# Performance work log

Hardware: AMD Instinct MI355X
Metric: run time of the kernel (lower is better)

## Reference

```python
import jax, jax.numpy as jnp
import numpy as np

N = 50000      # n_nodes
E = 800000     # n_edges (nnz)
F = 256        # n_features
H = 256        # architecture (GCN hidden)
K = 16         # n_clusters
CLUSTER_REG = 1.0
CON_REG = 1.0


def setup_inputs() -> dict:
    key = jax.random.key(0)
    ks = jax.random.split(key, 12)
    inp = {
        "edge_src": jax.random.randint(ks[0], (E,), 0, N, dtype=jnp.int32),
        "edge_dst": jax.random.randint(ks[1], (E,), 0, N, dtype=jnp.int32),
        "edge_w_norm": jax.random.uniform(ks[2], (E,), dtype=jnp.float32),
        "features": jax.random.normal(ks[3], (N, F), dtype=jnp.float32),
        "aug_features": jax.random.normal(ks[4], (N, F), dtype=jnp.float32),
        # GCN encoder params (Linear no-bias + additive bias per DGI-style GCN)
        "W1": jax.random.normal(ks[5], (F, H), dtype=jnp.float32) / np.sqrt(F),
        "b1": jnp.zeros((H,), dtype=jnp.float32),
        # student GCN params
        "Ws": jax.random.normal(ks[6], (H, K), dtype=jnp.float32) / np.sqrt(H),
        "bs": jnp.zeros((K,), dtype=jnp.float32),
        # teacher GCN params (EMA copy; fixed here)
        "Wt": jax.random.normal(ks[7], (H, K), dtype=jnp.float32) / np.sqrt(H),
        "bt": jnp.zeros((K,), dtype=jnp.float32),
        "n_nodes": N,
    }
    return inp


def _spmm(w, src, dst, X, n):
    # (sparse A) @ X with A given as COO (src=row, dst=col, w=value)
    return jax.ops.segment_sum(w[:, None] * X[dst], src, num_segments=n)


def _gcn(X, W, b, w, src, dst, n):
    # act(spmm(A_norm, X @ W) + b) with act = selu
    return jax.nn.selu(_spmm(w, src, dst, X @ W, n) + b)


def _normalize(x):
    # F.normalize(x, dim=-1, p=2)
    nrm = jnp.sqrt(jnp.sum(x * x, axis=-1, keepdims=True))
    return x / jnp.maximum(nrm, 1e-12)


def reference(edge_src, edge_dst, edge_w_norm, features, aug_features,
              W1, b1, Ws, bs, Wt, bt, n_nodes):
    n = features.shape[0]
    n_edges = edge_src.shape[0]

    # encoder + student assignments
    gcn_out = _gcn(features, W1, b1, edge_w_norm, edge_src, edge_dst, n)
    logits = _spmm(edge_w_norm, edge_src, edge_dst, gcn_out @ Ws, n) + bs
    assignments = jax.nn.softmax(jax.nn.selu(logits), axis=1)  # [N, K]

    # degrees = torch.sparse.sum(graph, dim=0) (binary adjacency values)
    ones_e = jnp.ones((n_edges,), dtype=features.dtype)
    degrees = jax.ops.segment_sum(ones_e, edge_dst, num_segments=n)[:, None]  # [N,1]

    # graph_pooled = (A @ S).T @ S  (A values are all 1)
    AS = jax.ops.segment_sum(assignments[edge_dst], edge_src, num_segments=n)
    graph_pooled = AS.T @ assignments  # [K, K]

    normalizer_left = assignments.T @ degrees          # [K, 1]
    normalizer = (normalizer_left @ normalizer_left.T) / 2.0 / n_edges
    spectral_loss = -jnp.trace(graph_pooled - normalizer) / 2.0 / n_edges

    cluster_sizes = jnp.sum(assignments, axis=0)
    cluster_loss = (jnp.linalg.norm(cluster_sizes) / n_nodes * np.sqrt(float(K)) - 1.0)
    cluster_loss = cluster_loss * CLUSTER_REG

    # teacher branch (no grad)
    g2 = _gcn(aug_features, W1, b1, edge_w_norm, edge_src, edge_dst, n)
    t_logits = _spmm(edge_w_norm, edge_src, edge_dst, g2 @ Wt, n) + bt
    assignments_hat = jax.lax.stop_gradient(
        jax.nn.softmax(jax.nn.selu(t_logits), axis=-1))

    con = jnp.mean(2.0 - 2.0 * jnp.sum(_normalize(assignments_hat) * _normalize(assignments), axis=-1))

    loss = spectral_loss + cluster_loss + CON_REG * con
    return loss
```

## Files before the change

kernel.cpp:

```cpp
#include <hip/hip_runtime.h>
#include <math.h>

constexpr int Fdim = 256;
constexpr int Hdim = 256;
constexpr int Kc   = 16;

constexpr int RSTRIDE = 32;
constexpr int NRED    = 34;
constexpr int BCAP    = 5120;

typedef __attribute__((ext_vector_type(8))) short s8v;
typedef __attribute__((ext_vector_type(4))) float f4v;

__device__ __forceinline__ float selu1(float x){
    const float scale = 1.0507009873554805f;
    const float alpha = 1.6732632423543772f;
    return scale * (x > 0.f ? x : alpha * expm1f(x));
}

__device__ __forceinline__ ushort f2bf(float x){
    union { float f; unsigned u; } c; c.f = x;
    unsigned r = c.u + 0x7fffu + ((c.u >> 16) & 1u);
    return (ushort)(r >> 16);
}

__device__ __forceinline__ float bflo(unsigned v){
    union { unsigned u; float f; } c; c.u = v << 16; return c.f;
}
__device__ __forceinline__ float bfhi(unsigned v){
    union { unsigned u; float f; } c; c.u = v & 0xffff0000u; return c.f;
}

__device__ __forceinline__ unsigned char f2fp8(float x){
    int v = __builtin_amdgcn_cvt_pk_fp8_f32(x, x, 0, false);
    return (unsigned char)(v & 0xff);
}

__global__ __launch_bounds__(256) void bin_kernel(
        const int* __restrict__ src, const int* __restrict__ dst,
        const float* __restrict__ w,
        int* __restrict__ bcnt,
        int* __restrict__ bsrc, uint2* __restrict__ bdw, int E, int nbuck){
    __shared__ int hist[256];
    __shared__ int base[256];
    __shared__ int cur[256];
    int t = threadIdx.x;
    int chunk = (E + gridDim.x - 1) / gridDim.x;
    int lo = blockIdx.x * chunk;
    int hi = min(lo + chunk, E);
    hist[t] = 0;
    __syncthreads();
    for (int i = lo + t; i < hi; i += 256)
        atomicAdd(&hist[src[i] >> 8], 1);
    __syncthreads();
    if (t < nbuck && hist[t] > 0)
        base[t] = atomicAdd(&bcnt[t * 32], hist[t]);
    cur[t] = 0;
    __syncthreads();
    for (int i = lo + t; i < hi; i += 256){
        int s = src[i], d = dst[i];
        float wv = w[i];
        int b = s >> 8;
        int p = base[b] + atomicAdd(&cur[b], 1);
        if (p < BCAP){
            bsrc[(size_t)b * BCAP + p] = s;
            bdw[(size_t)b * BCAP + p]  = make_uint2((unsigned)d, __float_as_uint(wv));
        }
    }
}

__global__ __launch_bounds__(256) void bbase_kernel(const int* __restrict__ bcnt,
        int* __restrict__ bbase, int* __restrict__ roff, int nbuck, int n){
    __shared__ int s[256];
    int t = threadIdx.x;
    int v = (t < nbuck) ? min(bcnt[t * 32], BCAP) : 0;
    s[t] = v;
    __syncthreads();
    for (int off = 1; off < 256; off <<= 1){
        int x = (t >= off) ? s[t - off] : 0;
        __syncthreads();
        s[t] += x;
        __syncthreads();
    }
    if (t < nbuck) bbase[t] = s[t] - v;
    if (t == 255) roff[n] = s[255];
}

__global__ __launch_bounds__(256) void csr_build_kernel(
        const int* __restrict__ bcnt, const int* __restrict__ bbase,
        const int* __restrict__ bsrc, const uint2* __restrict__ bdw,
        int* __restrict__ roff, uint2* __restrict__ csr, int n){
    __shared__ int hist[256];
    __shared__ int loc[256];
    __shared__ int cur[256];
    int b = blockIdx.x, t = threadIdx.x;
    int cnt  = min(bcnt[b * 32], BCAP);
    int base = bbase[b];
    hist[t] = 0;
    __syncthreads();
    for (int i = t; i < cnt; i += 256)
        atomicAdd(&hist[bsrc[(size_t)b * BCAP + i] & 255], 1);
    __syncthreads();
    int v = hist[t];
    loc[t] = v;
    __syncthreads();
    for (int off = 1; off < 256; off <<= 1){
        int x = (t >= off) ? loc[t - off] : 0;
        __syncthreads();
        loc[t] += x;
        __syncthreads();
    }
    int gi = b * 256 + t;
    if (gi < n) roff[gi] = base + loc[t] - v;
    cur[t] = 0;
    __syncthreads();
    for (int i = t; i < cnt; i += 256){
        int s   = bsrc[(size_t)b * BCAP + i];
        int idx = s & 255;
        int p = base + (loc[idx] - hist[idx]) + atomicAdd(&cur[idx], 1);
        csr[p] = bdw[(size_t)b * BCAP + i];
    }
}

__global__ void castw_kernel(const float* __restrict__ W, ushort* __restrict__ Wt){
    __shared__ float t[16][17];
    int tx = threadIdx.x, ty = threadIdx.y;
    int k  = blockIdx.y * 16 + ty;
    int nn = blockIdx.x * 16 + tx;
    t[ty][tx] = W[k * 256 + nn];
    __syncthreads();
    int n2 = blockIdx.x * 16 + ty;
    int k2 = blockIdx.y * 16 + tx;
    Wt[n2 * 256 + k2] = f2bf(t[tx][ty]);
}

__global__ void castwk_kernel(const float* __restrict__ Ws, const float* __restrict__ Wt,
                              ushort* __restrict__ WsT, ushort* __restrict__ WtT){
    int h = threadIdx.x;
    #pragma unroll
    for (int c = 0; c < 16; ++c){
        WsT[c * 256 + h] = f2bf(Ws[h * 16 + c]);
        WtT[c * 256 + h] = f2bf(Wt[h * 16 + c]);
    }
}

__global__ __launch_bounds__(256, 2) void gemm_xw_kernel(
        const float* __restrict__ A0, const float* __restrict__ A1,
        const ushort* __restrict__ Bt,
        unsigned char* __restrict__ C8, int M){
    __shared__ ushort blds[16384];
    int tid = threadIdx.x;
    int n0  = blockIdx.x * 128;
    int bm  = blockIdx.y * 128;
    const float* A = blockIdx.z ? A1 : A0;
    int halfoff = blockIdx.z * 256;

    int w = tid >> 6, l = tid & 63;
    int lr = l & 15, lk = l >> 4;

    int r0 = bm + w * 32 + lr;
    int r1 = r0 + 16;
    int rc0 = min(r0, M - 1), rc1 = min(r1, M - 1);

    f4v acc[2][8];
    #pragma unroll
    for (int m = 0; m < 2; ++m)
        #pragma unroll
        for (int t = 0; t < 8; ++t)
            acc[m][t] = (f4v){0.f, 0.f, 0.f, 0.f};

    for (int kp = 0; kp < 2; ++kp){
        #pragma unroll
        for (int j = 0; j < 8; ++j){
            int c  = j * 256 + tid;
            int nl = c >> 4, kc = c & 15;
            uint4 v = *reinterpret_cast<const uint4*>(
                Bt + (((size_t)(n0 + nl)) << 8) + kp * 128 + (kc << 3));
            unsigned boff = (unsigned)(((nl << 8) + (kc << 4)) ^ ((nl & 7) << 4));
            *reinterpret_cast<uint4*>(reinterpret_cast<char*>(blds) + boff) = v;
        }

        const float* a0 = A + (size_t)rc0 * 256 + kp * 128 + lk * 8;
        const float* a1 = A + (size_t)rc1 * 256 + kp * 128 + lk * 8;
        s8v af0[4], af1[4];
        #pragma unroll
        for (int ks = 0; ks < 4; ++ks){
            float4 x0 = *reinterpret_cast<const float4*>(a0 + ks * 32);
            float4 x1 = *reinterpret_cast<const float4*>(a0 + ks * 32 + 4);
            af0[ks][0] = (short)f2bf(x0.x); af0[ks][1] = (short)f2bf(x0.y);
            af0[ks][2] = (short)f2bf(x0.z); af0[ks][3] = (short)f2bf(x0.w);
            af0[ks][4] = (short)f2bf(x1.x); af0[ks][5] = (short)f2bf(x1.y);
            af0[ks][6] = (short)f2bf(x1.z); af0[ks][7] = (short)f2bf(x1.w);
            float4 y0 = *reinterpret_cast<const float4*>(a1 + ks * 32);
            float4 y1 = *reinterpret_cast<const float4*>(a1 + ks * 32 + 4);
            af1[ks][0] = (short)f2bf(y0.x); af1[ks][1] = (short)f2bf(y0.y);
            af1[ks][2] = (short)f2bf(y0.z); af1[ks][3] = (short)f2bf(y0.w);
            af1[ks][4] = (short)f2bf(y1.x); af1[ks][5] = (short)f2bf(y1.y);
            af1[ks][6] = (short)f2bf(y1.z); af1[ks][7] = (short)f2bf(y1.w);
        }
        __syncthreads();

        #pragma unroll
        for (int ks = 0; ks < 4; ++ks){
            #pragma unroll
            for (int t = 0; t < 8; ++t){
                int nl = t * 16 + lr;
                unsigned boff = (unsigned)(((nl << 8) + ((ks * 4 + lk) << 4)) ^ ((nl & 7) << 4));
                s8v bf = *reinterpret_cast<const s8v*>(reinterpret_cast<const char*>(blds) + boff);
                acc[0][t] = __builtin_amdgcn_mfma_f32_16x16x32_bf16(af0[ks], bf, acc[0][t], 0, 0, 0);
                acc[1][t] = __builtin_amdgcn_mfma_f32_16x16x32_bf16(af1[ks], bf, acc[1][t], 0, 0, 0);
            }
        }
        if (kp == 0) __syncthreads();
    }

    #pragma unroll
    for (int m = 0; m < 2; ++m){
        #pragma unroll
        for (int t = 0; t < 8; ++t){
            int col = n0 + t * 16 + lr;
            #pragma unroll
            for (int j = 0; j < 4; ++j){
                int row = bm + w * 32 + m * 16 + lk * 4 + j;
                if (row < M) C8[(size_t)row * 512 + halfoff + col] = f2fp8(acc[m][t][j]);
            }
        }
    }
}

__global__ __launch_bounds__(256) void spmm_h2_kernel(
        const unsigned char* __restrict__ XWp,
        const int* __restrict__ roff, const uint2* __restrict__ csr,
        const float* __restrict__ b1,
        ushort* __restrict__ Gs, ushort* __restrict__ Gt, int n){
    int wid = threadIdx.x >> 6, lane = threadIdx.x & 63;
    int r = blockIdx.x * 4 + wid;
    if (r >= n) return;
    int half = lane >> 5;
    int hl   = lane & 31;
    const unsigned char* base = XWp + lane * 8;
    int e0 = roff[r], e1 = roff[r + 1];
    float acc[8] = {};

    #define ACCUM8(V, W) do{                                                      \
        auto fa_ = __builtin_amdgcn_cvt_pk_f32_fp8((V).x, false);                 \
        acc[0] = fmaf((W), fa_[0], acc[0]); acc[1] = fmaf((W), fa_[1], acc[1]);   \
        auto fb_ = __builtin_amdgcn_cvt_pk_f32_fp8((V).x, true);                  \
        acc[2] = fmaf((W), fb_[0], acc[2]); acc[3] = fmaf((W), fb_[1], acc[3]);   \
        auto fc_ = __builtin_amdgcn_cvt_pk_f32_fp8((V).y, false);                 \
        acc[4] = fmaf((W), fc_[0], acc[4]); acc[5] = fmaf((W), fc_[1], acc[5]);   \
        auto fd_ = __builtin_amdgcn_cvt_pk_f32_fp8((V).y, true);                  \
        acc[6] = fmaf((W), fd_[0], acc[6]); acc[7] = fmaf((W), fd_[1], acc[7]);   \
    }while(0)

    int e = e0;
    for (; e + 7 < e1; e += 8){
        uint2 c0 = csr[e],     c1 = csr[e + 1];
        uint2 c2 = csr[e + 2], c3 = csr[e + 3];
        uint2 c4 = csr[e + 4], c5 = csr[e + 5];
        uint2 c6 = csr[e + 6], c7 = csr[e + 7];
        uint2 v0 = *reinterpret_cast<const uint2*>(base + ((size_t)c0.x << 9));
        uint2 v1 = *reinterpret_cast<const uint2*>(base + ((size_t)c1.x << 9));
        uint2 v2 = *reinterpret_cast<const uint2*>(base + ((size_t)c2.x << 9));
        uint2 v3 = *reinterpret_cast<const uint2*>(base + ((size_t)c3.x << 9));
        uint2 v4 = *reinterpret_cast<const uint2*>(base + ((size_t)c4.x << 9));
        uint2 v5 = *reinterpret_cast<const uint2*>(base + ((size_t)c5.x << 9));
        uint2 v6 = *reinterpret_cast<const uint2*>(base + ((size_t)c6.x << 9));
        uint2 v7 = *reinterpret_cast<const uint2*>(base + ((size_t)c7.x << 9));
        ACCUM8(v0, __uint_as_float(c0.y)); ACCUM8(v1, __uint_as_float(c1.y));
        ACCUM8(v2, __uint_as_float(c2.y)); ACCUM8(v3, __uint_as_float(c3.y));
        ACCUM8(v4, __uint_as_float(c4.y)); ACCUM8(v5, __uint_as_float(c5.y));
        ACCUM8(v6, __uint_as_float(c6.y)); ACCUM8(v7, __uint_as_float(c7.y));
    }
    for (; e + 3 < e1; e += 4){
        uint2 c0 = csr[e],     c1 = csr[e + 1];
        uint2 c2 = csr[e + 2], c3 = csr[e + 3];
        uint2 v0 = *reinterpret_cast<const uint2*>(base + ((size_t)c0.x << 9));
        uint2 v1 = *reinterpret_cast<const uint2*>(base + ((size_t)c1.x << 9));
        uint2 v2 = *reinterpret_cast<const uint2*>(base + ((size_t)c2.x << 9));
        uint2 v3 = *reinterpret_cast<const uint2*>(base + ((size_t)c3.x << 9));
        ACCUM8(v0, __uint_as_float(c0.y)); ACCUM8(v1, __uint_as_float(c1.y));
        ACCUM8(v2, __uint_as_float(c2.y)); ACCUM8(v3, __uint_as_float(c3.y));
    }
    for (; e < e1; ++e){
        uint2 c = csr[e];
        uint2 v = *reinterpret_cast<const uint2*>(base + ((size_t)c.x << 9));
        ACCUM8(v, __uint_as_float(c.y));
    }
    #undef ACCUM8

    const float* bp = b1 + hl * 8;
    float4 bb0 = *reinterpret_cast<const float4*>(bp);
    float4 bb1 = *reinterpret_cast<const float4*>(bp + 4);
    float bv[8] = {bb0.x, bb0.y, bb0.z, bb0.w, bb1.x, bb1.y, bb1.z, bb1.w};
    ushort o[8];
    #pragma unroll
    for (int q = 0; q < 8; ++q) o[q] = f2bf(selu1(acc[q] + bv[q]));
    uint4 ov = *reinterpret_cast<const uint4*>(o);
    ushort* gout = (half ? Gt : Gs) + (size_t)r * Hdim + hl * 8;
    *reinterpret_cast<uint4*>(gout) = ov;
}

__global__ __launch_bounds__(256) void gemm_k2_kernel(
        const ushort* __restrict__ Gs, const ushort* __restrict__ Gt,
        const ushort* __restrict__ WsT, const ushort* __restrict__ WtT,
        unsigned* __restrict__ GSp, int n){
    int wv = blockIdx.x * 4 + (threadIdx.x >> 6);
    int l  = threadIdx.x & 63;
    int lr = l & 15, lk = l >> 4;
    int nw = (n + 15) >> 4;
    if (wv >= nw) return;
    int r0 = wv * 16;

    s8v bs_[8], bt_[8];
    #pragma unroll
    for (int ks = 0; ks < 8; ++ks){
        bs_[ks] = *reinterpret_cast<const s8v*>(WsT + lr * 256 + ks * 32 + lk * 8);
        bt_[ks] = *reinterpret_cast<const s8v*>(WtT + lr * 256 + ks * 32 + lk * 8);
    }

    f4v accs = (f4v){0.f,0.f,0.f,0.f}, acct = (f4v){0.f,0.f,0.f,0.f};
    int row = min(r0 + lr, n - 1);
    const ushort* gsrow = Gs + (size_t)row * 256 + lk * 8;
    const ushort* gtrow = Gt + (size_t)row * 256 + lk * 8;
    #pragma unroll
    for (int ks = 0; ks < 8; ++ks){
        s8v a_s = *reinterpret_cast<const s8v*>(gsrow + ks * 32);
        s8v a_t = *reinterpret_cast<const s8v*>(gtrow + ks * 32);
        accs = __builtin_amdgcn_mfma_f32_16x16x32_bf16(a_s, bs_[ks], accs, 0, 0, 0);
        acct = __builtin_amdgcn_mfma_f32_16x16x32_bf16(a_t, bt_[ks], acct, 0, 0, 0);
    }
    #pragma unroll
    for (int j = 0; j < 4; ++j){
        int rr = r0 + lk * 4 + j;
        if (rr < n){
            unsigned pv = (unsigned)f2bf(accs[j]) | ((unsigned)f2bf(acct[j]) << 16);
            GSp[(size_t)rr * 16 + lr] = pv;
        }
    }
}

__global__ __launch_bounds__(256) void spmm_k2_kernel(
        const unsigned* __restrict__ GSp,
        const int* __restrict__ roff, const uint2* __restrict__ csr,
        const float* __restrict__ bsv, const float* __restrict__ btv,
        float* __restrict__ asg, float* __restrict__ red, int n){
    int tid  = threadIdx.x;
    int wid  = tid >> 6, lane = tid & 63;
    int slot = lane >> 4, j = lane & 15;
    float bs_ = bsv[j], bt_ = btv[j];
    float cs_l = 0.f, con_l = 0.f;

    int rstride = gridDim.x * 4;
    for (int r = blockIdx.x * 4 + wid; r < n; r += rstride){
        int e0 = roff[r], e1 = roff[r + 1];
        float as_ = 0.f, at_ = 0.f;
        for (int e = e0 + slot; e < e1; e += 4){
            uint2 c = csr[e];
            float w = __uint_as_float(c.y);
            unsigned v = GSp[(size_t)c.x * 16 + j];
            as_ = fmaf(w, bflo(v), as_);
            at_ = fmaf(w, bfhi(v), at_);
        }
        as_ += __shfl_xor(as_, 16); as_ += __shfl_xor(as_, 32);
        at_ += __shfl_xor(at_, 16); at_ += __shfl_xor(at_, 32);
        float xs = selu1(as_ + bs_);
        float xt = selu1(at_ + bt_);
        float ms = xs, mt = xt;
        #pragma unroll
        for (int off = 8; off >= 1; off >>= 1){
            ms = fmaxf(ms, __shfl_xor(ms, off));
            mt = fmaxf(mt, __shfl_xor(mt, off));
        }
        float es = expf(xs - ms), et = expf(xt - mt);
        float ss = es, st = et;
        #pragma unroll
        for (int off = 8; off >= 1; off >>= 1){
            ss += __shfl_xor(ss, off);
            st += __shfl_xor(st, off);
        }
        float a = es / ss, b = et / st;
        if (slot == 0) asg[(size_t)r * 16 + j] = a;
        cs_l += a;
        float dot = a * b, na = a * a, nb = b * b;
        #pragma unroll
        for (int off = 8; off >= 1; off >>= 1){
            dot += __shfl_xor(dot, off);
            na  += __shfl_xor(na, off);
            nb  += __shfl_xor(nb, off);
        }
        if (j == 0){
            na = fmaxf(sqrtf(na), 1e-12f);
            nb = fmaxf(sqrtf(nb), 1e-12f);
            con_l += 2.f - 2.f * dot / (na * nb);
        }
    }

    cs_l  += __shfl_xor(cs_l, 16);  cs_l  += __shfl_xor(cs_l, 32);  cs_l  *= 0.25f;
    con_l += __shfl_xor(con_l, 16); con_l += __shfl_xor(con_l, 32); con_l *= 0.25f;

    __shared__ float part[4][17];
    if (lane < 16) part[wid][lane] = cs_l;
    if (lane == 0) part[wid][16]   = con_l;
    __syncthreads();
    if (tid < 16){
        float s = part[0][tid] + part[1][tid] + part[2][tid] + part[3][tid];
        atomicAdd(&red[(16 + tid) * RSTRIDE], s);
    } else if (tid == 16){
        float s = part[0][16] + part[1][16] + part[2][16] + part[3][16];
        atomicAdd(&red[32 * RSTRIDE], s);
    }
}

__global__ __launch_bounds__(256) void edge_trace_kernel(const int* __restrict__ src,
        const int* __restrict__ dst, const float* __restrict__ as_,
        float* __restrict__ red, int E){
    int tid    = blockIdx.x * blockDim.x + threadIdx.x;
    int stride = gridDim.x * blockDim.x;
    float dot = 0.f;
    float nl[16] = {};
    for (int i = tid; i < E; i += stride){
        const float4* pa = reinterpret_cast<const float4*>(as_ + (size_t)src[i] * 16);
        const float4* pb = reinterpret_cast<const float4*>(as_ + (size_t)dst[i] * 16);
        #pragma unroll
        for (int q = 0; q < 4; ++q){
            float4 va = pa[q]; float4 vb = pb[q];
            dot = fmaf(va.x, vb.x, dot); dot = fmaf(va.y, vb.y, dot);
            dot = fmaf(va.z, vb.z, dot); dot = fmaf(va.w, vb.w, dot);
            nl[q*4+0] += vb.x; nl[q*4+1] += vb.y;
            nl[q*4+2] += vb.z; nl[q*4+3] += vb.w;
        }
    }
    #pragma unroll
    for (int off = 1; off < 64; off <<= 1){
        dot += __shfl_xor(dot, off);
        #pragma unroll
        for (int k = 0; k < 16; ++k) nl[k] += __shfl_xor(nl[k], off);
    }
    __shared__ float part[4][17];
    int wid = threadIdx.x >> 6, lane = threadIdx.x & 63;
    if (lane == 0){
        #pragma unroll
        for (int k = 0; k < 16; ++k) part[wid][k] = nl[k];
        part[wid][16] = dot;
    }
    __syncthreads();
    int t = threadIdx.x;
    if (t < 16){
        float s = part[0][t] + part[1][t] + part[2][t] + part[3][t];
        atomicAdd(&red[t * RSTRIDE], s);
    } else if (t == 16){
        float s = part[0][16] + part[1][16] + part[2][16] + part[3][16];
        atomicAdd(&red[33 * RSTRIDE], s);
    }
}

__global__ void finalize_kernel(const float* __restrict__ red, float* __restrict__ out,
                                int n, int E){
    float trace = red[33 * RSTRIDE];
    float nl2 = 0.f, cs2 = 0.f;
    #pragma unroll
    for (int k = 0; k < 16; ++k){
        nl2 = fmaf(red[k * RSTRIDE],        red[k * RSTRIDE],        nl2);
        cs2 = fmaf(red[(16 + k) * RSTRIDE], red[(16 + k) * RSTRIDE], cs2);
    }
    float twoE = 2.f * (float)E;
    float spectral = -(trace - nl2 / twoE) / twoE;
    float cluster  = sqrtf(cs2) / (float)n * 4.f - 1.f;
    float con      = red[32 * RSTRIDE] / (float)n;
    out[0] = spectral + cluster + con;
}

extern "C" void kernel_launch(void* const* d_in, const int* in_sizes, int n_in,
                              void* d_out, int out_size, void* d_ws, size_t ws_size,
                              hipStream_t stream){
    const int*   esrc = (const int*)d_in[0];
    const int*   edst = (const int*)d_in[1];
    const float* ew   = (const float*)d_in[2];
    const float* feat = (const float*)d_in[3];
    const float* faug = (const float*)d_in[4];
    const float* W1   = (const float*)d_in[5];
    const float* b1   = (const float*)d_in[6];
    const float* Wsm  = (const float*)d_in[7];
    const float* bsv  = (const float*)d_in[8];
    const float* Wtm  = (const float*)d_in[9];
    const float* btv  = (const float*)d_in[10];
    int E = in_sizes[0];
    int N = in_sizes[3] / Fdim;

    char* ws = (char*)d_ws;
    size_t off = 0;
    auto alloc = [&](size_t bytes) -> char* {
        char* p = ws + off;
        off = (off + bytes + 255) & ~(size_t)255;
        return p;
    };
    int nbuck = (N + 255) >> 8;
    unsigned char* XWp = (unsigned char*)alloc((size_t)N * 512);
    ushort*   Gs    = (ushort*)alloc((size_t)N * Hdim * 2);
    ushort*   Gt    = (ushort*)alloc((size_t)N * Hdim * 2);
    unsigned* GSp   = (unsigned*)alloc((size_t)N * Kc * 4);
    float*    ASG_S = (float*)alloc((size_t)N * Kc * 4);
    ushort*   WT    = (ushort*)alloc((size_t)256 * 256 * 2);
    ushort*   WsT   = (ushort*)alloc((size_t)16 * 256 * 2);
    ushort*   WtT   = (ushort*)alloc((size_t)16 * 256 * 2);
    int*      ROFF  = (int*)alloc((size_t)(N + 1) * 4);
    int*      BBASE = (int*)alloc((size_t)(nbuck + 1) * 4);
    int*      BCNT  = (int*)alloc((size_t)nbuck * 32 * 4);
    int*      BSRC  = (int*)alloc((size_t)nbuck * BCAP * 4);
    uint2*    BDW   = (uint2*)alloc((size_t)nbuck * BCAP * 8);
    uint2*    CSR8  = (uint2*)alloc((size_t)E * 8);
    float*    RED   = (float*)alloc((size_t)NRED * RSTRIDE * 4);

    hipMemsetAsync(BCNT, 0, (size_t)nbuck * 32 * 4, stream);
    hipMemsetAsync(RED, 0, (size_t)NRED * RSTRIDE * 4, stream);

    castw_kernel<<<dim3(16, 16), dim3(16, 16), 0, stream>>>(W1, WT);
    castwk_kernel<<<1, 256, 0, stream>>>(Wsm, Wtm, WsT, WtT);
    bin_kernel<<<256, 256, 0, stream>>>(esrc, edst, ew, BCNT, BSRC, BDW, E, nbuck);
    bbase_kernel<<<1, 256, 0, stream>>>(BCNT, BBASE, ROFF, nbuck, N);
    csr_build_kernel<<<nbuck, 256, 0, stream>>>(BCNT, BBASE, BSRC, BDW, ROFF, CSR8, N);

    dim3 gg(2, (N + 127) / 128, 2);
    gemm_xw_kernel<<<gg, 256, 0, stream>>>(feat, faug, WT, XWp, N);

    spmm_h2_kernel<<<(N + 3) / 4, 256, 0, stream>>>(XWp, ROFF, CSR8, b1, Gs, Gt, N);

    int nw = (N + 15) / 16;
    gemm_k2_kernel<<<(nw + 3) / 4, 256, 0, stream>>>(Gs, Gt, WsT, WtT, GSp, N);

    spmm_k2_kernel<<<2048, 256, 0, stream>>>(GSp, ROFF, CSR8, bsv, btv,
                                             ASG_S, RED, N);

    edge_trace_kernel<<<256, 256, 0, stream>>>(esrc, edst, ASG_S, RED, E);
    finalize_kernel<<<1, 1, 0, stream>>>(RED, (float*)d_out, N, E);
}
```

Before: 247.8 us.

## Merge edge binning with XW GEMM and fold bucket scan into CSR build

The two weight-cast kernels become one prep kernel. Edge binning and the feature GEMM now run as different block ranges of a single mega-kernel, so the bandwidth-bound binning can overlap with the MFMA GEMM. The bucket-base prefix scan is recomputed inside every CSR-build block, which removes a separate single-block kernel. This cuts the launch count from 6 to 3 in exchange for redundant scan work and a shared-memory footprint sized for the GEMM in all blocks.

```diff
diff --git a/kernel.cpp b/kernel.cpp
--- a/kernel.cpp
+++ b/kernel.cpp
@@ -36,124 +36,82 @@
     return (unsigned char)(v & 0xff);
 }
 
-__global__ __launch_bounds__(256) void bin_kernel(
-        const int* __restrict__ src, const int* __restrict__ dst,
-        const float* __restrict__ w,
-        int* __restrict__ bcnt,
-        int* __restrict__ bsrc, uint2* __restrict__ bdw, int E, int nbuck){
-    __shared__ int hist[256];
-    __shared__ int base[256];
-    __shared__ int cur[256];
+__global__ __launch_bounds__(256) void prep_kernel(
+        const float* __restrict__ W1, ushort* __restrict__ WT,
+        const float* __restrict__ Ws, const float* __restrict__ Wt,
+        ushort* __restrict__ WsT, ushort* __restrict__ WtT){
+    __shared__ float tbuf[16][17];
+    int b = blockIdx.x;
     int t = threadIdx.x;
-    int chunk = (E + gridDim.x - 1) / gridDim.x;
-    int lo = blockIdx.x * chunk;
-    int hi = min(lo + chunk, E);
-    hist[t] = 0;
-    __syncthreads();
-    for (int i = lo + t; i < hi; i += 256)
-        atomicAdd(&hist[src[i] >> 8], 1);
-    __syncthreads();
-    if (t < nbuck && hist[t] > 0)
-        base[t] = atomicAdd(&bcnt[t * 32], hist[t]);
-    cur[t] = 0;
-    __syncthreads();
-    for (int i = lo + t; i < hi; i += 256){
-        int s = src[i], d = dst[i];
-        float wv = w[i];
-        int b = s >> 8;
-        int p = base[b] + atomicAdd(&cur[b], 1);
-        if (p < BCAP){
-            bsrc[(size_t)b * BCAP + p] = s;
-            bdw[(size_t)b * BCAP + p]  = make_uint2((unsigned)d, __float_as_uint(wv));
-        }
-    }
-}
-
-__global__ __launch_bounds__(256) void bbase_kernel(const int* __restrict__ bcnt,
-        int* __restrict__ bbase, int* __restrict__ roff, int nbuck, int n){
-    __shared__ int s[256];
-    int t = threadIdx.x;
-    int v = (t < nbuck) ? min(bcnt[t * 32], BCAP) : 0;
-    s[t] = v;
-    __syncthreads();
-    for (int off = 1; off < 256; off <<= 1){
-        int x = (t >= off) ? s[t - off] : 0;
-        __syncthreads();
-        s[t] += x;
-        __syncthreads();
-    }
-    if (t < nbuck) bbase[t] = s[t] - v;
-    if (t == 255) roff[n] = s[255];
-}
-
-__global__ __launch_bounds__(256) void csr_build_kernel(
-        const int* __restrict__ bcnt, const int* __restrict__ bbase,
-        const int* __restrict__ bsrc, const uint2* __restrict__ bdw,
-        int* __restrict__ roff, uint2* __restrict__ csr, int n){
-    __shared__ int hist[256];
-    __shared__ int loc[256];
-    __shared__ int cur[256];
-    int b = blockIdx.x, t = threadIdx.x;
-    int cnt  = min(bcnt[b * 32], BCAP);
-    int base = bbase[b];
-    hist[t] = 0;
-    __syncthreads();
-    for (int i = t; i < cnt; i += 256)
-        atomicAdd(&hist[bsrc[(size_t)b * BCAP + i] & 255], 1);
-    __syncthreads();
-    int v = hist[t];
-    loc[t] = v;
-    __syncthreads();
-    for (int off = 1; off < 256; off <<= 1){
-        int x = (t >= off) ? loc[t - off] : 0;
-        __syncthreads();
-        loc[t] += x;
-        __syncthreads();
-    }
-    int gi = b * 256 + t;
-    if (gi < n) roff[gi] = base + loc[t] - v;
-    cur[t] = 0;
-    __syncthreads();
-    for (int i = t; i < cnt; i += 256){
-        int s   = bsrc[(size_t)b * BCAP + i];
-        int idx = s & 255;
-        int p = base + (loc[idx] - hist[idx]) + atomicAdd(&cur[idx], 1);
-        csr[p] = bdw[(size_t)b * BCAP + i];
-    }
-}
-
-__global__ void castw_kernel(const float* __restrict__ W, ushort* __restrict__ Wt){
-    __shared__ float t[16][17];
-    int tx = threadIdx.x, ty = threadIdx.y;
-    int k  = blockIdx.y * 16 + ty;
-    int nn = blockIdx.x * 16 + tx;
-    t[ty][tx] = W[k * 256 + nn];
-    __syncthreads();
-    int n2 = blockIdx.x * 16 + ty;
-    int k2 = blockIdx.y * 16 + tx;
-    Wt[n2 * 256 + k2] = f2bf(t[tx][ty]);
-}
-
-__global__ void castwk_kernel(const float* __restrict__ Ws, const float* __restrict__ Wt,
-                              ushort* __restrict__ WsT, ushort* __restrict__ WtT){
-    int h = threadIdx.x;
-    #pragma unroll
-    for (int c = 0; c < 16; ++c){
-        WsT[c * 256 + h] = f2bf(Ws[h * 16 + c]);
-        WtT[c * 256 + h] = f2bf(Wt[h * 16 + c]);
-    }
-}
-
-__global__ __launch_bounds__(256, 2) void gemm_xw_kernel(
+    if (b < 256){
+        int bx = b & 15, by = b >> 4;
+        int tx = t & 15, ty = t >> 4;
+        int k  = by * 16 + ty;
+        int nn = bx * 16 + tx;
+        tbuf[ty][tx] = W1[k * 256 + nn];
+        __syncthreads();
+        int n2 = bx * 16 + ty;
+        int k2 = by * 16 + tx;
+        WT[n2 * 256 + k2] = f2bf(tbuf[tx][ty]);
+    } else {
+        int h = t;
+        #pragma unroll
+        for (int c = 0; c < 16; ++c){
+            WsT[c * 256 + h] = f2bf(Ws[h * 16 + c]);
+            WtT[c * 256 + h] = f2bf(Wt[h * 16 + c]);
+        }
+    }
+}
+
+__global__ __launch_bounds__(256, 2) void mega_kernel(
+        const int* __restrict__ esrc, const int* __restrict__ edst,
+        const float* __restrict__ ew, int* __restrict__ bcnt,
+        int* __restrict__ bsrc, uint2* __restrict__ bdw, int E, int nbuck,
         const float* __restrict__ A0, const float* __restrict__ A1,
-        const ushort* __restrict__ Bt,
-        unsigned char* __restrict__ C8, int M){
-    __shared__ ushort blds[16384];
+        const ushort* __restrict__ Bt, unsigned char* __restrict__ C8,
+        int M, int nrt){
+    __shared__ char smem[32768];
     int tid = threadIdx.x;
-    int n0  = blockIdx.x * 128;
-    int bm  = blockIdx.y * 128;
-    const float* A = blockIdx.z ? A1 : A0;
-    int halfoff = blockIdx.z * 256;
+
+    if (blockIdx.x < 256){
+        int* hist = (int*)smem;
+        int* base = hist + 256;
+        int* cur  = base + 256;
+        int chunk = (E + 255) / 256;
+        int lo = blockIdx.x * chunk;
+        int hi = min(lo + chunk, E);
+        hist[tid] = 0;
+        __syncthreads();
+        for (int i = lo + tid; i < hi; i += 256)
+            atomicAdd(&hist[esrc[i] >> 8], 1);
+        __syncthreads();
+        if (tid < nbuck && hist[tid] > 0)
+            base[tid] = atomicAdd(&bcnt[tid * 32], hist[tid]);
+        cur[tid] = 0;
+        __syncthreads();
+        for (int i = lo + tid; i < hi; i += 256){
+            int s = esrc[i], d = edst[i];
+            float wv = ew[i];
+            int b = s >> 8;
+            int p = base[b] + atomicAdd(&cur[b], 1);
+            if (p < BCAP){
+                bsrc[(size_t)b * BCAP + p] = s;
+                bdw[(size_t)b * BCAP + p]  = make_uint2((unsigned)d, __float_as_uint(wv));
+            }
+        }
+        return;
+    }
+
+    ushort* blds = (ushort*)smem;
+    int gid = blockIdx.x - 256;
+    int z   = gid / (2 * nrt);
+    int rem = gid - z * (2 * nrt);
+    int by  = rem >> 1;
+    int bx  = rem & 1;
+    int n0  = bx * 128;
+    int bm  = by * 128;
+    const float* A = z ? A1 : A0;
+    int halfoff = z * 256;
 
     int w = tid >> 6, l = tid & 63;
     int lr = l & 15, lk = l >> 4;
@@ -225,6 +183,56 @@
                 if (row < M) C8[(size_t)row * 512 + halfoff + col] = f2fp8(acc[m][t][j]);
             }
         }
+    }
+}
+
+__global__ __launch_bounds__(256) void csr_build_kernel(
+        const int* __restrict__ bcnt,
+        const int* __restrict__ bsrc, const uint2* __restrict__ bdw,
+        int* __restrict__ roff, uint2* __restrict__ csr, int n, int nbuck){
+    __shared__ int sb[256];
+    __shared__ int hist[256];
+    __shared__ int loc[256];
+    __shared__ int cur[256];
+    int b = blockIdx.x, t = threadIdx.x;
+
+    int vb = (t < nbuck) ? min(bcnt[t * 32], BCAP) : 0;
+    sb[t] = vb;
+    __syncthreads();
+    for (int off = 1; off < 256; off <<= 1){
+        int x = (t >= off) ? sb[t - off] : 0;
+        __syncthreads();
+        sb[t] += x;
+        __syncthreads();
+    }
+    if (b == 0 && t == 0) roff[n] = sb[nbuck - 1];
+    int cnt  = min(bcnt[b * 32], BCAP);
+    int base = sb[b] - cnt;
+    __syncthreads();
+
+    hist[t] = 0;
+    __syncthreads();
+    for (int i = t; i < cnt; i += 256)
+        atomicAdd(&hist[bsrc[(size_t)b * BCAP + i] & 255], 1);
+    __syncthreads();
+    int v = hist[t];
+    loc[t] = v;
+    __syncthreads();
+    for (int off = 1; off < 256; off <<= 1){
+        int x = (t >= off) ? loc[t - off] : 0;
+        __syncthreads();
+        loc[t] += x;
+        __syncthreads();
+    }
+    int gi = b * 256 + t;
+    if (gi < n) roff[gi] = base + loc[t] - v;
+    cur[t] = 0;
+    __syncthreads();
+    for (int i = t; i < cnt; i += 256){
+        int s   = bsrc[(size_t)b * BCAP + i];
+        int idx = s & 255;
+        int p = base + (loc[idx] - hist[idx]) + atomicAdd(&cur[idx], 1);
+        csr[p] = bdw[(size_t)b * BCAP + i];
     }
 }
 
@@ -505,7 +513,6 @@
     ushort*   WsT   = (ushort*)alloc((size_t)16 * 256 * 2);
     ushort*   WtT   = (ushort*)alloc((size_t)16 * 256 * 2);
     int*      ROFF  = (int*)alloc((size_t)(N + 1) * 4);
-    int*      BBASE = (int*)alloc((size_t)(nbuck + 1) * 4);
     int*      BCNT  = (int*)alloc((size_t)nbuck * 32 * 4);
     int*      BSRC  = (int*)alloc((size_t)nbuck * BCAP * 4);
     uint2*    BDW   = (uint2*)alloc((size_t)nbuck * BCAP * 8);
@@ -515,14 +522,16 @@
     hipMemsetAsync(BCNT, 0, (size_t)nbuck * 32 * 4, stream);
     hipMemsetAsync(RED, 0, (size_t)NRED * RSTRIDE * 4, stream);
 
-    castw_kernel<<<dim3(16, 16), dim3(16, 16), 0, stream>>>(W1, WT);
-    castwk_kernel<<<1, 256, 0, stream>>>(Wsm, Wtm, WsT, WtT);
-    bin_kernel<<<256, 256, 0, stream>>>(esrc, edst, ew, BCNT, BSRC, BDW, E, nbuck);
-    bbase_kernel<<<1, 256, 0, stream>>>(BCNT, BBASE, ROFF, nbuck, N);
-    csr_build_kernel<<<nbuck, 256, 0, stream>>>(BCNT, BBASE, BSRC, BDW, ROFF, CSR8, N);
-
-    dim3 gg(2, (N + 127) / 128, 2);
-    gemm_xw_kernel<<<gg, 256, 0, stream>>>(feat, faug, WT, XWp, N);
+    prep_kernel<<<257, 256, 0, stream>>>(W1, WT, Wsm, Wtm, WsT, WtT);
+
+    int nrt = (N + 127) / 128;
+    int mega_blocks = 256 + 2 * nrt * 2;
+    mega_kernel<<<mega_blocks, 256, 0, stream>>>(esrc, edst, ew, BCNT, BSRC, BDW,
+                                                 E, nbuck, feat, faug, WT, XWp,
+                                                 N, nrt);
+
+    csr_build_kernel<<<nbuck, 256, 0, stream>>>(BCNT, BSRC, BDW, CSR8 ? ROFF : ROFF,
+                                                CSR8, N, nbuck);
 
     spmm_h2_kernel<<<(N + 3) / 4, 256, 0, stream>>>(XWp, ROFF, CSR8, b1, Gs, Gt, N);
 
```

Result: faster. 236.6 us (-4.5%).
